# Performance work log

Hardware: AMD Instinct MI355X
Metric: run time of the kernel (lower is better)

The kernel has to match this reference:

```python
import jax, jax.numpy as jnp
import numpy as np

F = 32        # nFilters
OPS = 5       # numOfOps (len(ratio))
CIN = 32      # in_planes of each filter's conv
N, H, W = 16, 128, 128
EPS = 1e-5    # BatchNorm2d default eps
RATIO = [0.3125, 0.3125, 0.1875, 0.125, 0.0625]


def setup_inputs() -> dict:
    key = jax.random.key(0)
    k1, k2 = jax.random.split(key, 2)
    x = jax.random.normal(k1, (N, CIN, H, W), jnp.float32)
    # each filter holds OPS weight variants (one per quantization op); 1 output channel each
    W_all = jax.random.normal(k2, (F, OPS, CIN, 3, 3), jnp.float32) * 0.05
    gamma = jnp.ones((F,), jnp.float32)
    beta = jnp.zeros((F,), jnp.float32)
    # setFiltersRatio: assign op index i to int(ratio[i]*F) consecutive filters
    counts = [int(r * F) for r in RATIO]
    counts[-1] = F - sum(counts[:-1])
    op_idx = jnp.asarray(np.repeat(np.arange(OPS), counts), jnp.int32)  # [F]
    return {"x": x, "W_all": W_all, "gamma": gamma, "beta": beta, "op_idx": op_idx}


def reference(x, W_all, gamma, beta, op_idx):
    # per-filter selection of the active op's conv weight (irregular gather)
    Wsel = W_all[jnp.arange(W_all.shape[0]), op_idx]  # [F, CIN, 3, 3]
    # all per-filter 1-out-channel convs of the same x == one grouped conv to F channels
    out1 = jax.lax.conv_general_dilated(
        x, Wsel, window_strides=(1, 1), padding="SAME",
        dimension_numbers=("NCHW", "OIHW", "NCHW"))  # [N, F, H, W]
    # BatchNorm2d in training mode: batch statistics over (N, H, W) per channel
    mean = out1.mean(axis=(0, 2, 3), keepdims=True)
    var = ((out1 - mean) ** 2).mean(axis=(0, 2, 3), keepdims=True)
    out1 = (out1 - mean) * jax.lax.rsqrt(var + EPS)
    out1 = out1 * gamma[None, :, None, None] + beta[None, :, None, None]
    # op[1] per filter: (quantized) ReLU activation — same math for every op variant
    return jax.nn.relu(out1)
```

## Files before the change

### kernel.cpp

```cpp
#include <hip/hip_runtime.h>

#define NB   16
#define CINC 32
#define HH   128
#define WWD  128
#define FF   32
#define OPSN 5
#define EPSV 1e-5f

#define WS_WFRAG_BOFF   262400
#define WS_XT_BOFF      280832
#define WS_NEED         (280832 + (size_t)16*130*130*32*2)

typedef __attribute__((ext_vector_type(8))) short bf16x8;
typedef __attribute__((ext_vector_type(4))) float f32x4;

__device__ __forceinline__ unsigned short f2bf(float f) {
    unsigned u = __builtin_bit_cast(unsigned, f);
    u += 0x7FFFu + ((u >> 16) & 1u);
    return (unsigned short)(u >> 16);
}
__device__ __forceinline__ unsigned pack2(float lo, float hi) {
    return (unsigned)f2bf(lo) | ((unsigned)f2bf(hi) << 16);
}

__global__ __launch_bounds__(256) void transform_kernel(
    const float* __restrict__ x, const float* __restrict__ Wall,
    const int* __restrict__ opidx, unsigned short* __restrict__ xt,
    unsigned short* __restrict__ wfrag, float* __restrict__ acc)
{
    __shared__ float lds[128 * 35];
    const int bid = blockIdx.x;
    const int tid = threadIdx.x;

    if (bid == NB * 130) {
        for (int i = tid; i < 1024; i += 256) acc[i] = 0.f;
        for (int idx = tid; idx < 9216; idx += 256) {
            int frag = idx >> 9;
            int lane = (idx >> 3) & 63;
            int j    = idx & 7;
            int s = frag >> 1, m = frag & 1;
            int kh = s / 3, kw = s - 3 * kh;
            int f = m * 16 + (lane & 15);
            int c = ((lane >> 4) << 3) + j;
            float v = Wall[((size_t)(f * OPSN + opidx[f]) * 288) + c * 9 + kh * 3 + kw];
            wfrag[idx] = f2bf(v);
        }
        return;
    }

    const int idx = bid >> 3;
    const int n   = (bid & 7) * 2 + (idx / 130);
    const int hp  = idx % 130;

    unsigned short* rowp = xt + (size_t)(n * 130 + hp) * 130 * 32;
    uint4 zz = make_uint4(0, 0, 0, 0);

    if (hp == 0 || hp == 129) {
        for (int c = tid; c < 520; c += 256) ((uint4*)rowp)[c] = zz;
        return;
    }

    const int h = hp - 1;
    const float* xr = x + ((size_t)n * CINC * HH + h) * WWD;
    const int c  = tid >> 3;
    const int wq = tid & 7;
#pragma unroll
    for (int it = 0; it < 4; ++it) {
        int w4 = wq + it * 8;
        float4 v = ((const float4*)(xr + (size_t)c * (HH * WWD)))[w4];
        int w = w4 * 4;
        lds[(w + 0) * 35 + c] = v.x;
        lds[(w + 1) * 35 + c] = v.y;
        lds[(w + 2) * 35 + c] = v.z;
        lds[(w + 3) * 35 + c] = v.w;
    }
    __syncthreads();
    for (int cc = tid; cc < 512; cc += 256) {
        int p = cc >> 2, k = cc & 3;
        const float* s = &lds[p * 35 + k * 8];
        uint4 o;
        o.x = pack2(s[0], s[1]); o.y = pack2(s[2], s[3]);
        o.z = pack2(s[4], s[5]); o.w = pack2(s[6], s[7]);
        ((uint4*)rowp)[4 + cc] = o;
    }
    if (tid < 4)       ((uint4*)rowp)[tid] = zz;
    else if (tid < 8)  ((uint4*)rowp)[129 * 4 + tid - 4] = zz;
}

#define LOADROW(f0, f1, f2, R)                                                  \
    {                                                                           \
        const unsigned short* rp =                                              \
            xbase + ((size_t)(R) * 130 + w0) * 32 + laneoff;                    \
        f0 = *(const bf16x8*)(rp);                                              \
        f1 = *(const bf16x8*)(rp + 32);                                         \
        f2 = *(const bf16x8*)(rp + 64);                                         \
    }

#define MROW(f0, f1, f2, aA, aB, kh)                                            \
    {                                                                           \
        aA = __builtin_amdgcn_mfma_f32_16x16x32_bf16(wfr[2*((kh)*3+0)],   f0, aA, 0,0,0); \
        aB = __builtin_amdgcn_mfma_f32_16x16x32_bf16(wfr[2*((kh)*3+0)+1], f0, aB, 0,0,0); \
        aA = __builtin_amdgcn_mfma_f32_16x16x32_bf16(wfr[2*((kh)*3+1)],   f1, aA, 0,0,0); \
        aB = __builtin_amdgcn_mfma_f32_16x16x32_bf16(wfr[2*((kh)*3+1)+1], f1, aB, 0,0,0); \
        aA = __builtin_amdgcn_mfma_f32_16x16x32_bf16(wfr[2*((kh)*3+2)],   f2, aA, 0,0,0); \
        aB = __builtin_amdgcn_mfma_f32_16x16x32_bf16(wfr[2*((kh)*3+2)+1], f2, aB, 0,0,0); \
    }

#define CONV_PROLOGUE                                                           \
    bf16x8 wfr[18];                                                             \
    _Pragma("unroll")                                                           \
    for (int i = 0; i < 18; ++i)                                                \
        wfr[i] = *(const bf16x8*)(wfrag + (i * 64 + lane) * 8);                 \
    const unsigned short* xbase = xt + (size_t)n * 130 * 130 * 32;              \
    const int laneoff = l15 * 32 + lhi * 8;                                     \
    f32x4 zz4 = {0.f, 0.f, 0.f, 0.f};                                           \
    f32x4 a0A = zz4, a0B = zz4, a1A = zz4, a1B = zz4;                           \
    f32x4 a2A = zz4, a2B = zz4, a3A = zz4, a3B = zz4;                           \
    bf16x8 c0, c1, c2, n0, n1, n2;                                              \
    LOADROW(c0, c1, c2, h0);                                                    \
    LOADROW(n0, n1, n2, h0 + 1);

#define CONV_BODY(FIN)                                                          \
    MROW(c0, c1, c2, a0A, a0B, 0);                                              \
    LOADROW(c0, c1, c2, h0 + 2);                                                \
    MROW(n0, n1, n2, a0A, a0B, 1);                                              \
    MROW(n0, n1, n2, a1A, a1B, 0);                                              \
    LOADROW(n0, n1, n2, h0 + 3);                                                \
    MROW(c0, c1, c2, a0A, a0B, 2);                                              \
    MROW(c0, c1, c2, a1A, a1B, 1);                                              \
    MROW(c0, c1, c2, a2A, a2B, 0);                                              \
    FIN(a0A, a0B, 0);                                                           \
    LOADROW(c0, c1, c2, h0 + 4);                                                \
    MROW(n0, n1, n2, a1A, a1B, 2);                                              \
    MROW(n0, n1, n2, a2A, a2B, 1);                                              \
    MROW(n0, n1, n2, a3A, a3B, 0);                                              \
    FIN(a1A, a1B, 1);                                                           \
    LOADROW(n0, n1, n2, h0 + 5);                                                \
    MROW(c0, c1, c2, a2A, a2B, 2);                                              \
    MROW(c0, c1, c2, a3A, a3B, 1);                                              \
    FIN(a2A, a2B, 2);                                                           \
    MROW(n0, n1, n2, a3A, a3B, 2);                                              \
    FIN(a3A, a3B, 3);

__global__ __launch_bounds__(256) void conv_stats_kernel(
    const unsigned short* __restrict__ xt,
    const unsigned short* __restrict__ wfrag,
    float* __restrict__ acc)
{
    __shared__ float red[4][64];
    const int bid  = blockIdx.x;
    const int tid  = threadIdx.x;
    const int n    = (bid & 7) * 2 + ((bid >> 3) & 1);
    const int rest = bid >> 4;
    const int h0   = (rest & 31) * 4;
    const int wh   = rest >> 5;
    const int lane = tid & 63;
    const int wv   = tid >> 6;
    const int w0   = wh * 64 + wv * 16;
    const int l15  = lane & 15, lhi = lane >> 4;

    float s8[8], q8[8];
#pragma unroll
    for (int j = 0; j < 8; ++j) { s8[j] = 0.f; q8[j] = 0.f; }

#define FIN_STATS(aA, aB, hh)                                                   \
    {                                                                           \
        _Pragma("unroll")                                                       \
        for (int r = 0; r < 4; ++r) {                                           \
            float v0 = aA[r], v1 = aB[r];                                       \
            s8[r]     += v0;  q8[r]     += v0 * v0;                             \
            s8[4 + r] += v1;  q8[4 + r] += v1 * v1;                             \
        }                                                                       \
    }

    CONV_PROLOGUE
    CONV_BODY(FIN_STATS)
#undef FIN_STATS

#pragma unroll
    for (int m = 1; m < 16; m <<= 1) {
#pragma unroll
        for (int j = 0; j < 8; ++j) {
            s8[j] += __shfl_xor(s8[j], m, 64);
            q8[j] += __shfl_xor(q8[j], m, 64);
        }
    }
    if (l15 == 0) {
#pragma unroll
        for (int j = 0; j < 8; ++j) {
            int f = (j < 4) ? (lhi * 4 + j) : (16 + lhi * 4 + (j - 4));
            red[wv][f]      = s8[j];
            red[wv][32 + f] = q8[j];
        }
    }
    __syncthreads();
    if (tid < 64) {
        float v = red[0][tid] + red[1][tid] + red[2][tid] + red[3][tid];
        atomicAdd(&acc[n * 64 + tid], v);
    }
}

__global__ __launch_bounds__(256) void conv_apply_kernel(
    const unsigned short* __restrict__ xt,
    const unsigned short* __restrict__ wfrag,
    const float* __restrict__ acc,
    const float* __restrict__ gamma, const float* __restrict__ beta,
    float* __restrict__ out)
{
    __shared__ float tot[64];
    __shared__ float bns[64];
    const int bid  = blockIdx.x;
    const int tid  = threadIdx.x;

    if (tid < 64) {
        float s = 0.f;
#pragma unroll
        for (int k = 0; k < 16; ++k) s += acc[k * 64 + tid];
        tot[tid] = s;
    }
    __syncthreads();
    if (tid < 32) {
        float cnt  = (float)(NB * HH * WWD);
        float mean = tot[tid] / cnt;
        float var  = tot[32 + tid] / cnt - mean * mean;
        float sc   = gamma[tid] * rsqrtf(var + EPSV);
        bns[tid]      = sc;
        bns[32 + tid] = beta[tid] - mean * sc;
    }

    const int n    = (bid & 7) * 2 + ((bid >> 3) & 1);
    const int rest = bid >> 4;
    const int h0   = (rest & 31) * 4;
    const int wh   = rest >> 5;
    const int lane = tid & 63;
    const int wv   = tid >> 6;
    const int w0   = wh * 64 + wv * 16;
    const int l15  = lane & 15, lhi = lane >> 4;

    __syncthreads();
    float sc0[4], sh0[4], sc1[4], sh1[4];
#pragma unroll
    for (int r = 0; r < 4; ++r) {
        int f0 = lhi * 4 + r, f1 = 16 + lhi * 4 + r;
        sc0[r] = bns[f0]; sh0[r] = bns[32 + f0];
        sc1[r] = bns[f1]; sh1[r] = bns[32 + f1];
    }

    float* ob = out + (size_t)(n * FF + lhi * 4) * (HH * WWD) + h0 * WWD + w0 + l15;

#define FIN_APPLY(aA, aB, hh)                                                   \
    {                                                                           \
        _Pragma("unroll")                                                       \
        for (int r = 0; r < 4; ++r) {                                           \
            __builtin_nontemporal_store(                                        \
                fmaxf(fmaf(aA[r], sc0[r], sh0[r]), 0.f),                        \
                ob + (size_t)r * (HH * WWD) + (hh) * WWD);                      \
            __builtin_nontemporal_store(                                        \
                fmaxf(fmaf(aB[r], sc1[r], sh1[r]), 0.f),                        \
                ob + (size_t)r * (HH * WWD) + 16 * (HH * WWD) + (hh) * WWD);    \
        }                                                                       \
    }

    CONV_PROLOGUE
    CONV_BODY(FIN_APPLY)
#undef FIN_APPLY
}

__global__ __launch_bounds__(256) void conv_kernel(
    const float* __restrict__ x, const float* __restrict__ Wall,
    const int* __restrict__ opidx, float* __restrict__ out)
{
    __shared__ float wlds[FF * 289];
    __shared__ float xlds[8 * 3 * 132];
    const int tid = threadIdx.x;
    const int h = blockIdx.x;
    const int n = blockIdx.y;
    for (int i = tid; i < FF * 288; i += 256) {
        int f = i / 288;
        int r = i - f * 288;
        int op = opidx[f];
        wlds[f * 289 + r] = Wall[(f * OPSN + op) * 288 + r];
    }
    const int f = tid & 31;
    const int wg = tid >> 5;
    const int w0 = wg << 4;
    float acc[16];
#pragma unroll
    for (int i = 0; i < 16; ++i) acc[i] = 0.f;
    const float* xn = x + (size_t)n * CINC * HH * WWD;
    for (int cc = 0; cc < 4; ++cc) {
        __syncthreads();
        for (int i = tid; i < 8 * 3 * 132; i += 256) {
            int c8 = i / (3 * 132);
            int rem = i - c8 * (3 * 132);
            int r = rem / 132;
            int wp = rem - r * 132;
            int hin = h + r - 1;
            int win = wp - 1;
            float v = 0.f;
            if ((unsigned)hin < HH && (unsigned)win < WWD)
                v = xn[((cc * 8 + c8) * HH + hin) * WWD + win];
            xlds[i] = v;
        }
        __syncthreads();
#pragma unroll
        for (int c8 = 0; c8 < 8; ++c8) {
            const int c = cc * 8 + c8;
            float wv[9];
#pragma unroll
            for (int k = 0; k < 9; ++k) wv[k] = wlds[f * 289 + c * 9 + k];
#pragma unroll
            for (int kh = 0; kh < 3; ++kh) {
                float xr[20];
                const float4* p = (const float4*)&xlds[(c8 * 3 + kh) * 132 + w0];
#pragma unroll
                for (int j = 0; j < 5; ++j) {
                    float4 v = p[j];
                    xr[j * 4 + 0] = v.x; xr[j * 4 + 1] = v.y;
                    xr[j * 4 + 2] = v.z; xr[j * 4 + 3] = v.w;
                }
#pragma unroll
                for (int kw = 0; kw < 3; ++kw) {
                    float wgt = wv[kh * 3 + kw];
#pragma unroll
                    for (int i = 0; i < 16; ++i)
                        acc[i] = fmaf(xr[i + kw], wgt, acc[i]);
                }
            }
        }
    }
    float* op_ = out + (((size_t)(n * FF + f) * HH + h) * WWD + w0);
#pragma unroll
    for (int j = 0; j < 4; ++j)
        ((float4*)op_)[j] = make_float4(acc[j * 4], acc[j * 4 + 1],
                                        acc[j * 4 + 2], acc[j * 4 + 3]);
}

__global__ __launch_bounds__(256) void stats_kernel(
    const float* __restrict__ out, const float* __restrict__ gamma,
    const float* __restrict__ beta, float* __restrict__ ws)
{
    __shared__ float ssum[256], ssq[256];
    const int f = blockIdx.x;
    const int tid = threadIdx.x;
    float s = 0.f, q = 0.f;
    for (int n = 0; n < NB; ++n) {
        const float4* p = (const float4*)(out + (size_t)(n * FF + f) * HH * WWD);
        for (int i = tid; i < HH * WWD / 4; i += 256) {
            float4 v = p[i];
            s += v.x + v.y + v.z + v.w;
            q += v.x * v.x + v.y * v.y + v.z * v.z + v.w * v.w;
        }
    }
    ssum[tid] = s; ssq[tid] = q;
    __syncthreads();
    for (int st = 128; st > 0; st >>= 1) {
        if (tid < st) { ssum[tid] += ssum[tid + st]; ssq[tid] += ssq[tid + st]; }
        __syncthreads();
    }
    if (tid == 0) {
        float cnt = (float)(NB * HH * WWD);
        float mean = ssum[0] / cnt;
        float var = ssq[0] / cnt - mean * mean;
        float sc = gamma[f] * rsqrtf(var + EPSV);
        ws[f] = sc;
        ws[FF + f] = beta[f] - mean * sc;
    }
}

__global__ __launch_bounds__(256) void apply_kernel(
    float* __restrict__ out, const float* __restrict__ bnp)
{
    const int total4 = NB * FF * HH * WWD / 4;
    for (int i = blockIdx.x * 256 + threadIdx.x; i < total4; i += gridDim.x * 256) {
        int f = (i >> 12) & 31;
        float sc = bnp[f], sh = bnp[FF + f];
        float4 v = ((const float4*)out)[i];
        v.x = fmaxf(fmaf(v.x, sc, sh), 0.f);
        v.y = fmaxf(fmaf(v.y, sc, sh), 0.f);
        v.z = fmaxf(fmaf(v.z, sc, sh), 0.f);
        v.w = fmaxf(fmaf(v.w, sc, sh), 0.f);
        ((float4*)out)[i] = v;
    }
}

extern "C" void kernel_launch(void* const* d_in, const int* in_sizes, int n_in,
                              void* d_out, int out_size, void* d_ws, size_t ws_size,
                              hipStream_t stream) {
    const float* x     = (const float*)d_in[0];
    const float* Wall  = (const float*)d_in[1];
    const float* gamma = (const float*)d_in[2];
    const float* beta  = (const float*)d_in[3];
    const int*   opidx = (const int*)d_in[4];
    float* out = (float*)d_out;
    float* ws  = (float*)d_ws;

    if (ws_size >= WS_NEED) {
        float*          acc   = ws;
        unsigned short* wfrag = (unsigned short*)((char*)d_ws + WS_WFRAG_BOFF);
        unsigned short* xt    = (unsigned short*)((char*)d_ws + WS_XT_BOFF);

        transform_kernel<<<NB * 130 + 1, 256, 0, stream>>>(x, Wall, opidx, xt, wfrag, acc);
        conv_stats_kernel<<<1024, 256, 0, stream>>>(xt, wfrag, acc);
        conv_apply_kernel<<<1024, 256, 0, stream>>>(xt, wfrag, acc, gamma, beta, out);
    } else {
        dim3 gridc(HH, NB);
        conv_kernel<<<gridc, 256, 0, stream>>>(x, Wall, opidx, out);
        stats_kernel<<<FF, 256, 0, stream>>>(out, gamma, beta, ws);
        apply_kernel<<<2048, 256, 0, stream>>>(out, ws);
    }
}
```

Before: 43.32 us.

## Store fp16 conv output in stats pass and stream-apply BN instead of recomputing conv

The stats pass now also writes the raw convolution result as fp16 into workspace. The final pass reads that buffer and applies batch-norm scale/shift plus ReLU with nontemporal stores, so the convolution is no longer recomputed a second time. This trades a second conv pass for an extra 16 MB of fp16 write and read traffic, and adds fp16 rounding of the pre-norm values. The path runs only when the workspace is large enough.

After: 56.54 us. +30.5%, slower.

```diff
diff --git a/kernel.cpp b/kernel.cpp
--- a/kernel.cpp
+++ b/kernel.cpp
@@ -10,7 +10,9 @@
 
 #define WS_WFRAG_BOFF   262400
 #define WS_XT_BOFF      280832
+#define WS_CO_BOFF      17586432
 #define WS_NEED         (280832 + (size_t)16*130*130*32*2)
+#define WS_NEED2        (WS_CO_BOFF + (size_t)NB*FF*HH*WWD*2)
 
 typedef __attribute__((ext_vector_type(8))) short bf16x8;
 typedef __attribute__((ext_vector_type(4))) float f32x4;
@@ -22,6 +24,13 @@
 }
 __device__ __forceinline__ unsigned pack2(float lo, float hi) {
     return (unsigned)f2bf(lo) | ((unsigned)f2bf(hi) << 16);
+}
+__device__ __forceinline__ unsigned short f2h(float f) {
+    _Float16 h = (_Float16)f;
+    return __builtin_bit_cast(unsigned short, h);
+}
+__device__ __forceinline__ float h2f(unsigned short u) {
+    return (float)__builtin_bit_cast(_Float16, u);
 }
 
 __global__ __launch_bounds__(256) void transform_kernel(
@@ -143,6 +152,124 @@
     MROW(n0, n1, n2, a3A, a3B, 2);                                              \
     FIN(a3A, a3B, 3);
 
+__global__ __launch_bounds__(256) void conv_stats_store_kernel(
+    const unsigned short* __restrict__ xt,
+    const unsigned short* __restrict__ wfrag,
+    float* __restrict__ acc, unsigned short* __restrict__ co)
+{
+    __shared__ float red[4][64];
+    const int bid  = blockIdx.x;
+    const int tid  = threadIdx.x;
+    const int n    = (bid & 7) * 2 + ((bid >> 3) & 1);
+    const int rest = bid >> 4;
+    const int h0   = (rest & 31) * 4;
+    const int wh   = rest >> 5;
+    const int lane = tid & 63;
+    const int wv   = tid >> 6;
+    const int w0   = wh * 64 + wv * 16;
+    const int l15  = lane & 15, lhi = lane >> 4;
+
+    float s8[8], q8[8];
+#pragma unroll
+    for (int j = 0; j < 8; ++j) { s8[j] = 0.f; q8[j] = 0.f; }
+
+    unsigned short* cb = co + (size_t)(n * FF + lhi * 4) * (HH * WWD)
+                            + h0 * WWD + w0 + l15;
+
+#define FIN_SS(aA, aB, hh)                                                      \
+    {                                                                           \
+        _Pragma("unroll")                                                       \
+        for (int r = 0; r < 4; ++r) {                                           \
+            float v0 = aA[r], v1 = aB[r];                                       \
+            s8[r]     += v0;  q8[r]     += v0 * v0;                             \
+            s8[4 + r] += v1;  q8[4 + r] += v1 * v1;                             \
+            cb[(size_t)r * (HH * WWD) + (hh) * WWD]                    = f2h(v0); \
+            cb[(size_t)r * (HH * WWD) + 16 * (HH * WWD) + (hh) * WWD]  = f2h(v1); \
+        }                                                                       \
+    }
+
+    CONV_PROLOGUE
+    CONV_BODY(FIN_SS)
+#undef FIN_SS
+
+#pragma unroll
+    for (int m = 1; m < 16; m <<= 1) {
+#pragma unroll
+        for (int j = 0; j < 8; ++j) {
+            s8[j] += __shfl_xor(s8[j], m, 64);
+            q8[j] += __shfl_xor(q8[j], m, 64);
+        }
+    }
+    if (l15 == 0) {
+#pragma unroll
+        for (int j = 0; j < 8; ++j) {
+            int f = (j < 4) ? (lhi * 4 + j) : (16 + lhi * 4 + (j - 4));
+            red[wv][f]      = s8[j];
+            red[wv][32 + f] = q8[j];
+        }
+    }
+    __syncthreads();
+    if (tid < 64) {
+        float v = red[0][tid] + red[1][tid] + red[2][tid] + red[3][tid];
+        atomicAdd(&acc[n * 64 + tid], v);
+    }
+}
+
+__global__ __launch_bounds__(256) void apply_stream_kernel(
+    const unsigned short* __restrict__ co, const float* __restrict__ acc,
+    const float* __restrict__ gamma, const float* __restrict__ beta,
+    float* __restrict__ out)
+{
+    __shared__ float tot[64];
+    __shared__ float bns[64];
+    const int tid = threadIdx.x;
+
+    if (tid < 64) {
+        float s = 0.f;
+#pragma unroll
+        for (int k = 0; k < 16; ++k) s += acc[k * 64 + tid];
+        tot[tid] = s;
+    }
+    __syncthreads();
+    if (tid < 32) {
+        float cnt  = (float)(NB * HH * WWD);
+        float mean = tot[tid] / cnt;
+        float var  = tot[32 + tid] / cnt - mean * mean;
+        float sc   = gamma[tid] * rsqrtf(var + EPSV);
+        bns[tid]      = sc;
+        bns[32 + tid] = beta[tid] - mean * sc;
+    }
+    __syncthreads();
+
+    const int i0 = (blockIdx.x * 256 + tid) * 16;
+    const int f  = (i0 >> 14) & 31;
+    const float sc = bns[f], sh = bns[32 + f];
+
+    uint4 a = *(const uint4*)(co + i0);
+    uint4 b = *(const uint4*)(co + i0 + 8);
+
+    float v[16];
+    v[0]  = h2f((unsigned short)(a.x & 0xffff)); v[1]  = h2f((unsigned short)(a.x >> 16));
+    v[2]  = h2f((unsigned short)(a.y & 0xffff)); v[3]  = h2f((unsigned short)(a.y >> 16));
+    v[4]  = h2f((unsigned short)(a.z & 0xffff)); v[5]  = h2f((unsigned short)(a.z >> 16));
+    v[6]  = h2f((unsigned short)(a.w & 0xffff)); v[7]  = h2f((unsigned short)(a.w >> 16));
+    v[8]  = h2f((unsigned short)(b.x & 0xffff)); v[9]  = h2f((unsigned short)(b.x >> 16));
+    v[10] = h2f((unsigned short)(b.y & 0xffff)); v[11] = h2f((unsigned short)(b.y >> 16));
+    v[12] = h2f((unsigned short)(b.z & 0xffff)); v[13] = h2f((unsigned short)(b.z >> 16));
+    v[14] = h2f((unsigned short)(b.w & 0xffff)); v[15] = h2f((unsigned short)(b.w >> 16));
+
+    f32x4* op = (f32x4*)(out + i0);
+#pragma unroll
+    for (int k = 0; k < 4; ++k) {
+        f32x4 o;
+        o.x = fmaxf(fmaf(v[4*k+0], sc, sh), 0.f);
+        o.y = fmaxf(fmaf(v[4*k+1], sc, sh), 0.f);
+        o.z = fmaxf(fmaf(v[4*k+2], sc, sh), 0.f);
+        o.w = fmaxf(fmaf(v[4*k+3], sc, sh), 0.f);
+        __builtin_nontemporal_store(o, op + k);
+    }
+}
+
 __global__ __launch_bounds__(256) void conv_stats_kernel(
     const unsigned short* __restrict__ xt,
     const unsigned short* __restrict__ wfrag,
@@ -396,7 +523,16 @@
     float* out = (float*)d_out;
     float* ws  = (float*)d_ws;
 
-    if (ws_size >= WS_NEED) {
+    if (ws_size >= WS_NEED2) {
+        float*          acc   = ws;
+        unsigned short* wfrag = (unsigned short*)((char*)d_ws + WS_WFRAG_BOFF);
+        unsigned short* xt    = (unsigned short*)((char*)d_ws + WS_XT_BOFF);
+        unsigned short* co    = (unsigned short*)((char*)d_ws + WS_CO_BOFF);
+
+        transform_kernel<<<NB * 130 + 1, 256, 0, stream>>>(x, Wall, opidx, xt, wfrag, acc);
+        conv_stats_store_kernel<<<1024, 256, 0, stream>>>(xt, wfrag, acc, co);
+        apply_stream_kernel<<<2048, 256, 0, stream>>>(co, acc, gamma, beta, out);
+    } else if (ws_size >= WS_NEED) {
         float*          acc   = ws;
         unsigned short* wfrag = (unsigned short*)((char*)d_ws + WS_WFRAG_BOFF);
         unsigned short* xt    = (unsigned short*)((char*)d_ws + WS_XT_BOFF);
```
